# Kernel tuning notes

Hardware: AMD Instinct MI355X
Metric: run time of the kernel (lower is better)

Reference implementation:

```python
import jax, jax.numpy as jnp
import numpy as np

N = 50000
D_IN = 512
D_OUT = 512
NUM_SAMPLE = 2


def setup_inputs() -> dict:
    key = jax.random.key(0)
    ks = jax.random.split(key, 8)
    x = jax.random.normal(ks[0], (N, D_IN), dtype=jnp.float32)
    neighs1 = jax.random.randint(ks[1], (N, NUM_SAMPLE), 0, N, dtype=jnp.int32)
    neighs2 = jax.random.randint(ks[2], (N, NUM_SAMPLE), 0, N, dtype=jnp.int32)
    # SageLayer weights: [out, 2*in] (self || aggregated neighbors), xavier-ish scale
    W1 = jax.random.normal(ks[3], (D_OUT, 2 * D_IN), dtype=jnp.float32) * 0.03
    W2 = jax.random.normal(ks[4], (D_OUT, 2 * D_OUT), dtype=jnp.float32) * 0.03
    fc_w = jax.random.normal(ks[5], (2, N * D_OUT), dtype=jnp.float32) * 0.0005
    fc_b = jnp.zeros((2,), dtype=jnp.float32)
    return {"x": x, "neighs1": neighs1, "neighs2": neighs2,
            "W1": W1, "W2": W2, "fc_w": fc_w, "fc_b": fc_b}


def _sage_layer(h, neighs, W):
    # MEAN aggregation over the num_sample sampled neighbors (self excluded, gcn=False).
    # Equivalent to the original dense one-hot mask.div(num_neigh).mm(embed_matrix).
    agg = h[neighs].mean(axis=1)                      # [N, S, d] -> [N, d]
    combined = jnp.concatenate([h, agg], axis=1)      # [N, 2d]
    # F.relu(W.mm(combined.t())).t() == relu(combined @ W.T)
    return jax.nn.relu(combined @ W.T)                # [N, out]


def reference(x, neighs1, neighs2, W1, W2, fc_w, fc_b):
    h = _sage_layer(x, neighs1, W1)
    h = _sage_layer(h, neighs2, W2)
    flat = h.reshape(1, -1)                           # [1, N*out]
    logits = flat @ fc_w.T + fc_b                     # [1, 2]
    return (flat, jax.nn.log_softmax(logits, axis=1))
```

## Files before the change

kernel.cpp:

```cpp
#include <hip/hip_runtime.h>
#include <stdint.h>

typedef short bf16x8 __attribute__((ext_vector_type(8)));
typedef float f32x4 __attribute__((ext_vector_type(4)));
typedef unsigned short u16x8 __attribute__((ext_vector_type(8)));

#define N_NODES 50000
#define DIM 512
#define TDIM 1024
#define NPAD 50048
#define M_TILES 391
#define GEMM_GRID 3136
#define FLAT_TOTAL 25600000ULL
#define NBLK_COMB 12500

__device__ __forceinline__ unsigned short f2bf(float f) {
    unsigned u = __float_as_uint(f);
    unsigned r = u + 0x7FFFu + ((u >> 16) & 1u);
    return (unsigned short)(r >> 16);
}
__device__ __forceinline__ float bf2f(unsigned short h) {
    return __uint_as_float(((unsigned)h) << 16);
}

__device__ __forceinline__ void llds16(const void* g, void* l) {
    __builtin_amdgcn_global_load_lds(
        (const __attribute__((address_space(1))) void*)g,
        (__attribute__((address_space(3))) void*)l,
        16, 0, 0);
}

__global__ void cast_x(const float* __restrict__ x, unsigned short* __restrict__ o) {
    size_t i = ((size_t)blockIdx.x * blockDim.x + threadIdx.x) * 8;
    float4 v0 = *(const float4*)&x[i];
    float4 v1 = *(const float4*)&x[i + 4];
    u16x8 r;
    r[0] = f2bf(v0.x); r[1] = f2bf(v0.y); r[2] = f2bf(v0.z); r[3] = f2bf(v0.w);
    r[4] = f2bf(v1.x); r[5] = f2bf(v1.y); r[6] = f2bf(v1.z); r[7] = f2bf(v1.w);
    *(u16x8*)&o[i] = r;
}

__global__ void cast_w_split2(const float* __restrict__ w1, const float* __restrict__ w2,
                              unsigned short* __restrict__ o1, unsigned short* __restrict__ o2) {
    int b = blockIdx.x;
    const float* w = (b < 256) ? w1 : w2;
    unsigned short* o = (b < 256) ? o1 : o2;
    int idx = ((b & 255) * 256 + threadIdx.x) * 8;
    int j = idx >> 9;
    int k = idx & 511;
    size_t src = (j < 512) ? ((size_t)j * 1024 + k) : ((size_t)(j - 512) * 1024 + 512 + k);
    float4 v0 = *(const float4*)&w[src];
    float4 v1 = *(const float4*)&w[src + 4];
    u16x8 r;
    r[0] = f2bf(v0.x); r[1] = f2bf(v0.y); r[2] = f2bf(v0.z); r[3] = f2bf(v0.w);
    r[4] = f2bf(v1.x); r[5] = f2bf(v1.y); r[6] = f2bf(v1.z); r[7] = f2bf(v1.w);
    *(u16x8*)&o[idx] = r;
}

__global__ __launch_bounds__(256)
void gemm_nt(const unsigned short* __restrict__ A, const unsigned short* __restrict__ B,
             unsigned short* __restrict__ T) {
    __shared__ unsigned short As[2][128 * 32];
    __shared__ unsigned short Bs[2][128 * 32];

    int x = blockIdx.x & 7;
    int g = blockIdx.x >> 3;
    int bm = x + 8 * (g >> 3);
    int bn = g & 7;
    if (bm >= M_TILES) return;

    int t = threadIdx.x;
    int lane = t & 63;
    int wave = t >> 6;
    int m_off = (wave >> 1) * 64;
    int n_off = (wave & 1) * 64;
    int lrow = lane & 15;
    int lk = (lane >> 4) * 8;

    f32x4 acc[4][4];
#pragma unroll
    for (int i = 0; i < 4; i++)
#pragma unroll
        for (int j = 0; j < 4; j++) acc[i][j] = (f32x4){0.f, 0.f, 0.f, 0.f};

    const unsigned short* ga = A + (size_t)(bm * 128 + (t >> 2)) * DIM + (t & 3) * 8;
    const unsigned short* gb = B + (size_t)(bn * 128 + (t >> 2)) * DIM + (t & 3) * 8;

    for (int k0 = 0; k0 < DIM; k0 += 64) {
        __syncthreads();
        llds16(ga + k0,            &As[0][t * 8]);
        llds16(ga + k0 + 64 * DIM, &As[0][t * 8 + 2048]);
        llds16(gb + k0,            &Bs[0][t * 8]);
        llds16(gb + k0 + 64 * DIM, &Bs[0][t * 8 + 2048]);
        llds16(ga + k0 + 32,            &As[1][t * 8]);
        llds16(ga + k0 + 32 + 64 * DIM, &As[1][t * 8 + 2048]);
        llds16(gb + k0 + 32,            &Bs[1][t * 8]);
        llds16(gb + k0 + 32 + 64 * DIM, &Bs[1][t * 8 + 2048]);
        __syncthreads();

#pragma unroll
        for (int h = 0; h < 2; h++) {
            bf16x8 af[4], bfr[4];
#pragma unroll
            for (int i = 0; i < 4; i++)
                af[i] = *(const bf16x8*)&As[h][(m_off + i * 16 + lrow) * 32 + lk];
#pragma unroll
            for (int j = 0; j < 4; j++)
                bfr[j] = *(const bf16x8*)&Bs[h][(n_off + j * 16 + lrow) * 32 + lk];
#pragma unroll
            for (int i = 0; i < 4; i++)
#pragma unroll
                for (int j = 0; j < 4; j++)
                    acc[i][j] = __builtin_amdgcn_mfma_f32_16x16x32_bf16(af[i], bfr[j], acc[i][j], 0, 0, 0);
        }
    }

    int lc = lane & 15;
    int lr = (lane >> 4) << 2;
#pragma unroll
    for (int i = 0; i < 4; i++) {
        int row0 = bm * 128 + m_off + i * 16 + lr;
#pragma unroll
        for (int j = 0; j < 4; j++) {
            int col = bn * 128 + n_off + j * 16 + lc;
            f32x4 v = acc[i][j];
#pragma unroll
            for (int r = 0; r < 4; r++)
                T[(size_t)(row0 + r) * TDIM + col] = f2bf(v[r]);
        }
    }
}

__global__ void combine1(const unsigned short* __restrict__ T, const int* __restrict__ nb,
                         unsigned short* __restrict__ H) {
    int t = threadIdx.x;
    int i = blockIdx.x * 4 + (t >> 6);
    int lane = t & 63;
    int c = lane * 8;
    int n0 = nb[i * 2], n1 = nb[i * 2 + 1];
    u16x8 p  = *(const u16x8*)&T[(size_t)i  * TDIM + c];
    u16x8 q0 = *(const u16x8*)&T[(size_t)n0 * TDIM + 512 + c];
    u16x8 q1 = *(const u16x8*)&T[(size_t)n1 * TDIM + 512 + c];
    u16x8 o;
#pragma unroll
    for (int j = 0; j < 8; j++)
        o[j] = f2bf(fmaxf(bf2f(p[j]) + 0.5f * (bf2f(q0[j]) + bf2f(q1[j])), 0.f));
    *(u16x8*)&H[(size_t)i * DIM + c] = o;
}

__global__ void combine2(const unsigned short* __restrict__ T, const int* __restrict__ nb,
                         const float* __restrict__ fcw, float* __restrict__ out,
                         float2* __restrict__ partials) {
    int t = threadIdx.x;
    int i = blockIdx.x * 4 + (t >> 6);
    int lane = t & 63;
    int w = t >> 6;
    int c = lane * 8;
    int n0 = nb[i * 2], n1 = nb[i * 2 + 1];
    u16x8 p  = *(const u16x8*)&T[(size_t)i  * TDIM + c];
    u16x8 q0 = *(const u16x8*)&T[(size_t)n0 * TDIM + 512 + c];
    u16x8 q1 = *(const u16x8*)&T[(size_t)n1 * TDIM + 512 + c];
    float v[8];
#pragma unroll
    for (int j = 0; j < 8; j++)
        v[j] = fmaxf(bf2f(p[j]) + 0.5f * (bf2f(q0[j]) + bf2f(q1[j])), 0.f);
    size_t ob = (size_t)i * DIM + c;
    *(float4*)&out[ob]     = (float4){v[0], v[1], v[2], v[3]};
    *(float4*)&out[ob + 4] = (float4){v[4], v[5], v[6], v[7]};
    float4 a0 = *(const float4*)&fcw[ob];
    float4 a1 = *(const float4*)&fcw[ob + 4];
    float4 b0 = *(const float4*)&fcw[FLAT_TOTAL + ob];
    float4 b1 = *(const float4*)&fcw[FLAT_TOTAL + ob + 4];
    float s0 = v[0]*a0.x + v[1]*a0.y + v[2]*a0.z + v[3]*a0.w
             + v[4]*a1.x + v[5]*a1.y + v[6]*a1.z + v[7]*a1.w;
    float s1 = v[0]*b0.x + v[1]*b0.y + v[2]*b0.z + v[3]*b0.w
             + v[4]*b1.x + v[5]*b1.y + v[6]*b1.z + v[7]*b1.w;
#pragma unroll
    for (int off = 32; off > 0; off >>= 1) {
        s0 += __shfl_down(s0, off);
        s1 += __shfl_down(s1, off);
    }
    __shared__ float r0[4], r1[4];
    if (lane == 0) { r0[w] = s0; r1[w] = s1; }
    __syncthreads();
    if (t == 0)
        partials[blockIdx.x] = make_float2(r0[0] + r0[1] + r0[2] + r0[3],
                                           r1[0] + r1[1] + r1[2] + r1[3]);
}

__global__ void reduce_finalize(const float2* __restrict__ partials, const float* __restrict__ fcb,
                                float* __restrict__ out2) {
    float s0 = 0.f, s1 = 0.f;
    for (int k = threadIdx.x; k < NBLK_COMB; k += 1024) {
        float2 pr = partials[k];
        s0 += pr.x; s1 += pr.y;
    }
#pragma unroll
    for (int off = 32; off > 0; off >>= 1) {
        s0 += __shfl_down(s0, off);
        s1 += __shfl_down(s1, off);
    }
    __shared__ float r0[16], r1[16];
    int lane = threadIdx.x & 63, w = threadIdx.x >> 6;
    if (lane == 0) { r0[w] = s0; r1[w] = s1; }
    __syncthreads();
    if (threadIdx.x == 0) {
        float l0 = fcb[0], l1 = fcb[1];
#pragma unroll
        for (int k = 0; k < 16; k++) { l0 += r0[k]; l1 += r1[k]; }
        float m = fmaxf(l0, l1);
        float lse = m + logf(expf(l0 - m) + expf(l1 - m));
        out2[0] = l0 - lse;
        out2[1] = l1 - lse;
    }
}

extern "C" void kernel_launch(void* const* d_in, const int* in_sizes, int n_in,
                              void* d_out, int out_size, void* d_ws, size_t ws_size,
                              hipStream_t stream) {
    const float* x   = (const float*)d_in[0];
    const int*   n1  = (const int*)d_in[1];
    const int*   n2  = (const int*)d_in[2];
    const float* W1  = (const float*)d_in[3];
    const float* W2  = (const float*)d_in[4];
    const float* fcw = (const float*)d_in[5];
    const float* fcb = (const float*)d_in[6];
    float* out = (float*)d_out;

    char* ws = (char*)d_ws;
    const size_t XB_OFF  = 0;
    const size_t T_OFF   = XB_OFF + (size_t)NPAD * DIM * 2;
    const size_t H1_OFF  = T_OFF + (size_t)NPAD * TDIM * 2;
    const size_t W1_OFF  = H1_OFF + (size_t)NPAD * DIM * 2;
    const size_t W2_OFF  = W1_OFF + (size_t)TDIM * DIM * 2;
    const size_t P_OFF   = W2_OFF + (size_t)TDIM * DIM * 2;
    unsigned short* Xb  = (unsigned short*)(ws + XB_OFF);
    unsigned short* T   = (unsigned short*)(ws + T_OFF);
    unsigned short* H1  = (unsigned short*)(ws + H1_OFF);
    unsigned short* W1s = (unsigned short*)(ws + W1_OFF);
    unsigned short* W2s = (unsigned short*)(ws + W2_OFF);
    float2* partials    = (float2*)(ws + P_OFF);

    cast_w_split2<<<512, 256, 0, stream>>>(W1, W2, W1s, W2s);
    cast_x<<<12500, 256, 0, stream>>>(x, Xb);

    gemm_nt<<<GEMM_GRID, 256, 0, stream>>>(Xb, W1s, T);
    combine1<<<NBLK_COMB, 256, 0, stream>>>(T, n1, H1);
    gemm_nt<<<GEMM_GRID, 256, 0, stream>>>(H1, W2s, T);
    combine2<<<NBLK_COMB, 256, 0, stream>>>(T, n2, fcw, out, partials);

    reduce_finalize<<<1, 1024, 0, stream>>>(partials, fcb, out + FLAT_TOTAL);
}
```

Baseline: 553.8 us.

## Aggregate neighbors before GEMM and fuse ReLU and FC reduction into epilogue

The neighbor mean is now taken on the inputs and written into the second half of a concatenated [h, agg] buffer. Each layer then becomes a single K=1024 GEMM with a 512-wide output, instead of a 1024-wide product followed by a gather-combine pass. ReLU is applied in the GEMM epilogue. The second layer's epilogue also writes the fp32 output and computes the two FC dot-product partials, which removes both combine kernels and the large intermediate T buffer. The trade-offs are that the epilogue now does scalar, less coalesced fp32 stores and fcw loads, and the gathers run on bf16 inputs before the GEMM.

New measurement: 665.1 us. 20.1% more time.

```diff
diff --git a/kernel.cpp b/kernel.cpp
--- a/kernel.cpp
+++ b/kernel.cpp
@@ -7,12 +7,12 @@
 
 #define N_NODES 50000
 #define DIM 512
-#define TDIM 1024
+#define KDIM 1024
 #define NPAD 50048
 #define M_TILES 391
-#define GEMM_GRID 3136
+#define GEMM_GRID 1568
 #define FLAT_TOTAL 25600000ULL
-#define NBLK_COMB 12500
+#define NBLK_AGG 12500
 
 __device__ __forceinline__ unsigned short f2bf(float f) {
     unsigned u = __float_as_uint(f);
@@ -30,44 +30,64 @@
         16, 0, 0);
 }
 
-__global__ void cast_x(const float* __restrict__ x, unsigned short* __restrict__ o) {
-    size_t i = ((size_t)blockIdx.x * blockDim.x + threadIdx.x) * 8;
-    float4 v0 = *(const float4*)&x[i];
-    float4 v1 = *(const float4*)&x[i + 4];
+__global__ void cast_x(const float* __restrict__ x, unsigned short* __restrict__ XA) {
+    size_t idx = ((size_t)blockIdx.x * blockDim.x + threadIdx.x) * 8;
+    float4 v0 = *(const float4*)&x[idx];
+    float4 v1 = *(const float4*)&x[idx + 4];
     u16x8 r;
     r[0] = f2bf(v0.x); r[1] = f2bf(v0.y); r[2] = f2bf(v0.z); r[3] = f2bf(v0.w);
     r[4] = f2bf(v1.x); r[5] = f2bf(v1.y); r[6] = f2bf(v1.z); r[7] = f2bf(v1.w);
-    *(u16x8*)&o[i] = r;
-}
-
-__global__ void cast_w_split2(const float* __restrict__ w1, const float* __restrict__ w2,
-                              unsigned short* __restrict__ o1, unsigned short* __restrict__ o2) {
+    size_t row = idx >> 9;
+    size_t col = idx & 511;
+    *(u16x8*)&XA[row * KDIM + col] = r;
+}
+
+__global__ void cast_w2(const float* __restrict__ w1, const float* __restrict__ w2,
+                        unsigned short* __restrict__ o1, unsigned short* __restrict__ o2) {
     int b = blockIdx.x;
     const float* w = (b < 256) ? w1 : w2;
     unsigned short* o = (b < 256) ? o1 : o2;
     int idx = ((b & 255) * 256 + threadIdx.x) * 8;
-    int j = idx >> 9;
-    int k = idx & 511;
-    size_t src = (j < 512) ? ((size_t)j * 1024 + k) : ((size_t)(j - 512) * 1024 + 512 + k);
-    float4 v0 = *(const float4*)&w[src];
-    float4 v1 = *(const float4*)&w[src + 4];
+    float4 v0 = *(const float4*)&w[idx];
+    float4 v1 = *(const float4*)&w[idx + 4];
     u16x8 r;
     r[0] = f2bf(v0.x); r[1] = f2bf(v0.y); r[2] = f2bf(v0.z); r[3] = f2bf(v0.w);
     r[4] = f2bf(v1.x); r[5] = f2bf(v1.y); r[6] = f2bf(v1.z); r[7] = f2bf(v1.w);
     *(u16x8*)&o[idx] = r;
 }
 
+__global__ void agg_mean(unsigned short* __restrict__ buf, const int* __restrict__ nb) {
+    int t = threadIdx.x;
+    int i = blockIdx.x * 4 + (t >> 6);
+    int lane = t & 63;
+    int c = lane * 8;
+    int n0 = nb[i * 2], n1 = nb[i * 2 + 1];
+    u16x8 a = *(const u16x8*)&buf[(size_t)n0 * KDIM + c];
+    u16x8 b = *(const u16x8*)&buf[(size_t)n1 * KDIM + c];
+    u16x8 o;
+#pragma unroll
+    for (int j = 0; j < 8; j++)
+        o[j] = f2bf(0.5f * (bf2f(a[j]) + bf2f(b[j])));
+    *(u16x8*)&buf[(size_t)i * KDIM + 512 + c] = o;
+}
+
+template <int EPI>
 __global__ __launch_bounds__(256)
 void gemm_nt(const unsigned short* __restrict__ A, const unsigned short* __restrict__ B,
-             unsigned short* __restrict__ T) {
+             unsigned short* __restrict__ H, const float* __restrict__ fcw,
+             float* __restrict__ out, float2* __restrict__ partials) {
     __shared__ unsigned short As[2][128 * 32];
     __shared__ unsigned short Bs[2][128 * 32];
+    __shared__ float r0[4], r1[4];
 
     int x = blockIdx.x & 7;
     int g = blockIdx.x >> 3;
-    int bm = x + 8 * (g >> 3);
-    int bn = g & 7;
-    if (bm >= M_TILES) return;
+    int bm = x + 8 * (g >> 2);
+    int bn = g & 3;
+    if (bm >= M_TILES) {
+        if (EPI == 2 && threadIdx.x == 0) partials[blockIdx.x] = make_float2(0.f, 0.f);
+        return;
+    }
 
     int t = threadIdx.x;
     int lane = t & 63;
@@ -83,19 +103,19 @@
 #pragma unroll
         for (int j = 0; j < 4; j++) acc[i][j] = (f32x4){0.f, 0.f, 0.f, 0.f};
 
-    const unsigned short* ga = A + (size_t)(bm * 128 + (t >> 2)) * DIM + (t & 3) * 8;
-    const unsigned short* gb = B + (size_t)(bn * 128 + (t >> 2)) * DIM + (t & 3) * 8;
-
-    for (int k0 = 0; k0 < DIM; k0 += 64) {
+    const unsigned short* ga = A + (size_t)(bm * 128 + (t >> 2)) * KDIM + (t & 3) * 8;
+    const unsigned short* gb = B + (size_t)(bn * 128 + (t >> 2)) * KDIM + (t & 3) * 8;
+
+    for (int k0 = 0; k0 < KDIM; k0 += 64) {
         __syncthreads();
-        llds16(ga + k0,            &As[0][t * 8]);
-        llds16(ga + k0 + 64 * DIM, &As[0][t * 8 + 2048]);
-        llds16(gb + k0,            &Bs[0][t * 8]);
-        llds16(gb + k0 + 64 * DIM, &Bs[0][t * 8 + 2048]);
-        llds16(ga + k0 + 32,            &As[1][t * 8]);
-        llds16(ga + k0 + 32 + 64 * DIM, &As[1][t * 8 + 2048]);
-        llds16(gb + k0 + 32,            &Bs[1][t * 8]);
-        llds16(gb + k0 + 32 + 64 * DIM, &Bs[1][t * 8 + 2048]);
+        llds16(ga + k0,             &As[0][t * 8]);
+        llds16(ga + k0 + 64 * KDIM, &As[0][t * 8 + 2048]);
+        llds16(gb + k0,             &Bs[0][t * 8]);
+        llds16(gb + k0 + 64 * KDIM, &Bs[0][t * 8 + 2048]);
+        llds16(ga + k0 + 32,             &As[1][t * 8]);
+        llds16(ga + k0 + 32 + 64 * KDIM, &As[1][t * 8 + 2048]);
+        llds16(gb + k0 + 32,             &Bs[1][t * 8]);
+        llds16(gb + k0 + 32 + 64 * KDIM, &Bs[1][t * 8 + 2048]);
         __syncthreads();
 
 #pragma unroll
@@ -117,81 +137,59 @@
 
     int lc = lane & 15;
     int lr = (lane >> 4) << 2;
-#pragma unroll
-    for (int i = 0; i < 4; i++) {
-        int row0 = bm * 128 + m_off + i * 16 + lr;
-#pragma unroll
-        for (int j = 0; j < 4; j++) {
-            int col = bn * 128 + n_off + j * 16 + lc;
-            f32x4 v = acc[i][j];
-#pragma unroll
-            for (int r = 0; r < 4; r++)
-                T[(size_t)(row0 + r) * TDIM + col] = f2bf(v[r]);
-        }
-    }
-}
-
-__global__ void combine1(const unsigned short* __restrict__ T, const int* __restrict__ nb,
-                         unsigned short* __restrict__ H) {
-    int t = threadIdx.x;
-    int i = blockIdx.x * 4 + (t >> 6);
-    int lane = t & 63;
-    int c = lane * 8;
-    int n0 = nb[i * 2], n1 = nb[i * 2 + 1];
-    u16x8 p  = *(const u16x8*)&T[(size_t)i  * TDIM + c];
-    u16x8 q0 = *(const u16x8*)&T[(size_t)n0 * TDIM + 512 + c];
-    u16x8 q1 = *(const u16x8*)&T[(size_t)n1 * TDIM + 512 + c];
-    u16x8 o;
-#pragma unroll
-    for (int j = 0; j < 8; j++)
-        o[j] = f2bf(fmaxf(bf2f(p[j]) + 0.5f * (bf2f(q0[j]) + bf2f(q1[j])), 0.f));
-    *(u16x8*)&H[(size_t)i * DIM + c] = o;
-}
-
-__global__ void combine2(const unsigned short* __restrict__ T, const int* __restrict__ nb,
-                         const float* __restrict__ fcw, float* __restrict__ out,
-                         float2* __restrict__ partials) {
-    int t = threadIdx.x;
-    int i = blockIdx.x * 4 + (t >> 6);
-    int lane = t & 63;
-    int w = t >> 6;
-    int c = lane * 8;
-    int n0 = nb[i * 2], n1 = nb[i * 2 + 1];
-    u16x8 p  = *(const u16x8*)&T[(size_t)i  * TDIM + c];
-    u16x8 q0 = *(const u16x8*)&T[(size_t)n0 * TDIM + 512 + c];
-    u16x8 q1 = *(const u16x8*)&T[(size_t)n1 * TDIM + 512 + c];
-    float v[8];
-#pragma unroll
-    for (int j = 0; j < 8; j++)
-        v[j] = fmaxf(bf2f(p[j]) + 0.5f * (bf2f(q0[j]) + bf2f(q1[j])), 0.f);
-    size_t ob = (size_t)i * DIM + c;
-    *(float4*)&out[ob]     = (float4){v[0], v[1], v[2], v[3]};
-    *(float4*)&out[ob + 4] = (float4){v[4], v[5], v[6], v[7]};
-    float4 a0 = *(const float4*)&fcw[ob];
-    float4 a1 = *(const float4*)&fcw[ob + 4];
-    float4 b0 = *(const float4*)&fcw[FLAT_TOTAL + ob];
-    float4 b1 = *(const float4*)&fcw[FLAT_TOTAL + ob + 4];
-    float s0 = v[0]*a0.x + v[1]*a0.y + v[2]*a0.z + v[3]*a0.w
-             + v[4]*a1.x + v[5]*a1.y + v[6]*a1.z + v[7]*a1.w;
-    float s1 = v[0]*b0.x + v[1]*b0.y + v[2]*b0.z + v[3]*b0.w
-             + v[4]*b1.x + v[5]*b1.y + v[6]*b1.z + v[7]*b1.w;
-#pragma unroll
-    for (int off = 32; off > 0; off >>= 1) {
-        s0 += __shfl_down(s0, off);
-        s1 += __shfl_down(s1, off);
-    }
-    __shared__ float r0[4], r1[4];
-    if (lane == 0) { r0[w] = s0; r1[w] = s1; }
-    __syncthreads();
-    if (t == 0)
-        partials[blockIdx.x] = make_float2(r0[0] + r0[1] + r0[2] + r0[3],
-                                           r1[0] + r1[1] + r1[2] + r1[3]);
+
+    if (EPI == 1) {
+#pragma unroll
+        for (int i = 0; i < 4; i++) {
+            int row0 = bm * 128 + m_off + i * 16 + lr;
+#pragma unroll
+            for (int j = 0; j < 4; j++) {
+                int col = bn * 128 + n_off + j * 16 + lc;
+                f32x4 v = acc[i][j];
+#pragma unroll
+                for (int r = 0; r < 4; r++)
+                    H[(size_t)(row0 + r) * KDIM + col] = f2bf(fmaxf(v[r], 0.f));
+            }
+        }
+    } else {
+        float s0 = 0.f, s1 = 0.f;
+#pragma unroll
+        for (int i = 0; i < 4; i++) {
+            int row0 = bm * 128 + m_off + i * 16 + lr;
+#pragma unroll
+            for (int j = 0; j < 4; j++) {
+                int col = bn * 128 + n_off + j * 16 + lc;
+                f32x4 v = acc[i][j];
+#pragma unroll
+                for (int r = 0; r < 4; r++) {
+                    int row = row0 + r;
+                    if (row < N_NODES) {
+                        float vv = fmaxf(v[r], 0.f);
+                        size_t off = (size_t)row * DIM + col;
+                        out[off] = vv;
+                        s0 += vv * fcw[off];
+                        s1 += vv * fcw[FLAT_TOTAL + off];
+                    }
+                }
+            }
+        }
+#pragma unroll
+        for (int off = 32; off > 0; off >>= 1) {
+            s0 += __shfl_down(s0, off);
+            s1 += __shfl_down(s1, off);
+        }
+        if (lane == 0) { r0[wave] = s0; r1[wave] = s1; }
+        __syncthreads();
+        if (t == 0)
+            partials[blockIdx.x] = make_float2(r0[0] + r0[1] + r0[2] + r0[3],
+                                               r1[0] + r1[1] + r1[2] + r1[3]);
+    }
 }
 
 __global__ void reduce_finalize(const float2* __restrict__ partials, const float* __restrict__ fcb,
                                 float* __restrict__ out2) {
     float s0 = 0.f, s1 = 0.f;
-    for (int k = threadIdx.x; k < NBLK_COMB; k += 1024) {
+    for (int k = threadIdx.x; k < GEMM_GRID; k += 1024) {
         float2 pr = partials[k];
         s0 += pr.x; s1 += pr.y;
     }
@@ -228,26 +226,24 @@
     float* out = (float*)d_out;
 
     char* ws = (char*)d_ws;
-    const size_t XB_OFF  = 0;
-    const size_t T_OFF   = XB_OFF + (size_t)NPAD * DIM * 2;
-    const size_t H1_OFF  = T_OFF + (size_t)NPAD * TDIM * 2;
-    const size_t W1_OFF  = H1_OFF + (size_t)NPAD * DIM * 2;
-    const size_t W2_OFF  = W1_OFF + (size_t)TDIM * DIM * 2;
-    const size_t P_OFF   = W2_OFF + (size_t)TDIM * DIM * 2;
-    unsigned short* Xb  = (unsigned short*)(ws + XB_OFF);
-    unsigned short* T   = (unsigned short*)(ws + T_OFF);
-    unsigned short* H1  = (unsigned short*)(ws + H1_OFF);
-    unsigned short* W1s = (unsigned short*)(ws + W1_OFF);
-    unsigned short* W2s = (unsigned short*)(ws + W2_OFF);
+    const size_t XA_OFF = 0;
+    const size_t HA_OFF = XA_OFF + (size_t)NPAD * KDIM * 2;
+    const size_t W1_OFF = HA_OFF + (size_t)NPAD * KDIM * 2;
+    const size_t W2_OFF = W1_OFF + (size_t)DIM * KDIM * 2;
+    const size_t P_OFF  = W2_OFF + (size_t)DIM * KDIM * 2;
+    unsigned short* XA  = (unsigned short*)(ws + XA_OFF);
+    unsigned short* HA  = (unsigned short*)(ws + HA_OFF);
+    unsigned short* W1r = (unsigned short*)(ws + W1_OFF);
+    unsigned short* W2r = (unsigned short*)(ws + W2_OFF);
     float2* partials    = (float2*)(ws + P_OFF);
 
-    cast_w_split2<<<512, 256, 0, stream>>>(W1, W2, W1s, W2s);
-    cast_x<<<12500, 256, 0, stream>>>(x, Xb);
-
-    gemm_nt<<<GEMM_GRID, 256, 0, stream>>>(Xb, W1s, T);
-    combine1<<<NBLK_COMB, 256, 0, stream>>>(T, n1, H1);
-    gemm_nt<<<GEMM_GRID, 256, 0, stream>>>(H1, W2s, T);
-    combine2<<<NBLK_COMB, 256, 0, stream>>>(T, n2, fcw, out, partials);
+    cast_w2<<<512, 256, 0, stream>>>(W1, W2, W1r, W2r);
+    cast_x<<<12500, 256, 0, stream>>>(x, XA);
+
+    agg_mean<<<NBLK_AGG, 256, 0, stream>>>(XA, n1);
+    gemm_nt<1><<<GEMM_GRID, 256, 0, stream>>>(XA, W1r, HA, nullptr, nullptr, nullptr);
+    agg_mean<<<NBLK_AGG, 256, 0, stream>>>(HA, n2);
+    gemm_nt<2><<<GEMM_GRID, 256, 0, stream>>>(HA, W2r, nullptr, fcw, out, partials);
 
     reduce_finalize<<<1, 1024, 0, stream>>>(partials, fcb, out + FLAT_TOTAL);
 }
```
